# Performance work log

Measured on AMD Instinct MI355X. Metric: run time of the kernel, lower is better.

## Reference

```python
import jax, jax.numpy as jnp
import numpy as np

B, T, E, H = 4, 1024, 512, 8


def setup_inputs() -> dict:
    key = jax.random.key(0)
    ks = jax.random.split(key, 8)
    s = 1.0 / np.sqrt(E)
    return {
        "x": jax.random.normal(ks[0], (B, T, E), dtype=jnp.float32),
        "mask": jnp.zeros((B, T, T), dtype=jnp.float32),
        "Wk": jax.random.uniform(ks[1], (H * E, E), minval=-s, maxval=s, dtype=jnp.float32),
        "Wq": jax.random.uniform(ks[2], (H * E, E), minval=-s, maxval=s, dtype=jnp.float32),
        "Wv": jax.random.uniform(ks[3], (H * E, E), minval=-s, maxval=s, dtype=jnp.float32),
        "Wu": jax.random.uniform(ks[4], (E, H * E), minval=-s, maxval=s, dtype=jnp.float32),
        "bu": jnp.zeros((E,), dtype=jnp.float32),
        "heads": H,
    }


def reference(x, mask, Wk, Wq, Wv, Wu, bu, heads):
    b, t, e = x.shape
    h = heads
    # Projections: torch Linear computes x @ W.T; output features laid out as [h, e]
    k = (x @ Wk.T).reshape(b, t, h, e).transpose(0, 2, 1, 3)  # [b,h,t,e]
    q = (x @ Wq.T).reshape(b, t, h, e).transpose(0, 2, 1, 3)
    v = (x @ Wv.T).reshape(b, t, h, e).transpose(0, 2, 1, 3)
    dot = jnp.einsum("bhqe,bhke->bhqk", q, k) / jnp.sqrt(jnp.float32(e))
    # mask repeat_interleave over b*h == broadcast over heads; subtracted additively
    att = jax.nn.softmax(dot - mask[:, None, :, :], axis=-1)
    out = jnp.einsum("bhqk,bhke->bhqe", att, v)  # [b,h,t,e]
    out = out.transpose(0, 2, 1, 3).reshape(b, t, h * e)
    return out @ Wu.T + bu
```

## Files before the change

### kernel.cpp

```cpp
#include <hip/hip_runtime.h>
#include <hip/hip_bf16.h>


typedef short bf16x8 __attribute__((ext_vector_type(8)));
typedef float f32x4 __attribute__((ext_vector_type(4)));
typedef unsigned short u16x8 __attribute__((ext_vector_type(8)));

__device__ __forceinline__ unsigned short f2bf(float f) {
  unsigned int u = __float_as_uint(f);
  u += 0x7FFFu + ((u >> 16) & 1u);
  return (unsigned short)(u >> 16);
}
__device__ __forceinline__ float bf2f(unsigned short s) {
  return __uint_as_float(((unsigned int)s) << 16);
}

typedef const __attribute__((address_space(1))) unsigned int* gas1_t;
typedef __attribute__((address_space(3))) unsigned int* las3_t;

__device__ __forceinline__ void gload16(const unsigned short* g, unsigned short* l) {
  __builtin_amdgcn_global_load_lds((gas1_t)g, (las3_t)l, 16, 0, 0);
}

__device__ __forceinline__ void store_val(unsigned short* p, float v) { *p = f2bf(v); }
__device__ __forceinline__ void store_val(float* p, float v) { *p = v; }

template<typename OutT>
__global__ __launch_bounds__(512, 1) void gemm_bt2(
    const unsigned short* __restrict__ A, const unsigned short* __restrict__ B,
    OutT* __restrict__ C,
    int K, int lda, int ldb, int ldc, int zshift,
    long long sAb, long long sAh, long long sBb, long long sBh,
    long long sCb, long long sCh, float alpha)
{
  const int tid  = threadIdx.x;
  const int lane = tid & 63;
  const int wave = tid >> 6;
  const int l15 = lane & 15, lhi = lane >> 4;
  const int wm = wave >> 2, wn = wave & 3;

  const int nx = gridDim.x, nxy = gridDim.x * gridDim.y;
  const int nwg = nxy * gridDim.z;
  int flat = blockIdx.x + nx * blockIdx.y + nxy * blockIdx.z;
  flat = (flat & 7) * (nwg >> 3) + (flat >> 3);
  const int bz = flat / nxy;
  const int rem = flat - bz * nxy;
  const int by = rem / nx;
  const int bx = rem - by * nx;

  const int bb = bz >> zshift, hh = bz & ((1 << zshift) - 1);
  const long long m0 = (long long)by * 256;
  const long long n0 = (long long)bx * 256;

  const unsigned short* Ab = A + bb * sAb + hh * sAh;
  const unsigned short* Bb = B + bb * sBb + hh * sBh;

  __shared__ __align__(16) unsigned short lds[49152];

  const unsigned short* gA[2];
  const unsigned short* gB[2];
  int fidx[2];
#pragma unroll
  for (int c = 0; c < 2; ++c) {
    const int f = c * 8 + wave;
    fidx[c] = f;
    gA[c] = Ab + (size_t)(m0 + f * 16 + l15) * lda + lhi * 8;
    gB[c] = Bb + (size_t)(n0 + f * 16 + l15) * ldb + lhi * 8;
  }

  auto stage = [&](int n, int p) {
    unsigned short* dst = lds + p * 16384;
    const int ko = n * 32;
#pragma unroll
    for (int c = 0; c < 2; ++c) {
      gload16(gA[c] + ko, dst + fidx[c] * 512);
      gload16(gB[c] + ko, dst + 8192 + fidx[c] * 512);
    }
  };

  f32x4 acc[8][4];
#pragma unroll
  for (int m = 0; m < 8; ++m)
#pragma unroll
    for (int n = 0; n < 4; ++n) acc[m][n] = (f32x4){0.f, 0.f, 0.f, 0.f};

  const int nt = K >> 5;
  stage(0, 0);
  stage(1, 1);
  asm volatile("s_waitcnt vmcnt(4)" ::: "memory");
  __builtin_amdgcn_sched_barrier(0);
  __builtin_amdgcn_s_barrier();

  for (int t = 0; t < nt; ++t) {
    const bool pref = (t + 2 < nt);
    if (pref) stage(t + 2, (t + 2) % 3);
    const unsigned short* base = lds + (t % 3) * 16384;
    bf16x8 af[8], bf[4];
#pragma unroll
    for (int mf = 0; mf < 8; ++mf)
      af[mf] = *(const bf16x8*)(base + (wm * 8 + mf) * 512 + lane * 8);
#pragma unroll
    for (int nf = 0; nf < 4; ++nf)
      bf[nf] = *(const bf16x8*)(base + 8192 + (wn * 4 + nf) * 512 + lane * 8);
    __builtin_amdgcn_s_setprio(1);
#pragma unroll
    for (int mf = 0; mf < 8; ++mf)
#pragma unroll
      for (int nf = 0; nf < 4; ++nf)
        acc[mf][nf] = __builtin_amdgcn_mfma_f32_16x16x32_bf16(af[mf], bf[nf], acc[mf][nf], 0, 0, 0);
    __builtin_amdgcn_s_setprio(0);
    if (pref) asm volatile("s_waitcnt vmcnt(4)" ::: "memory");
    else      asm volatile("s_waitcnt vmcnt(0)" ::: "memory");
    __builtin_amdgcn_sched_barrier(0);
    __builtin_amdgcn_s_barrier();
    __builtin_amdgcn_sched_barrier(0);
  }

  OutT* Cb = C + bb * sCb + hh * sCh;
#pragma unroll
  for (int mf = 0; mf < 8; ++mf) {
#pragma unroll
    for (int nf = 0; nf < 4; ++nf) {
      const long long col = n0 + wn * 64 + nf * 16 + l15;
#pragma unroll
      for (int r = 0; r < 4; ++r) {
        const long long row = m0 + wm * 128 + mf * 16 + lhi * 4 + r;
        store_val(Cb + (size_t)row * ldc + col, acc[mf][nf][r] * alpha);
      }
    }
  }
}

__global__ __launch_bounds__(256) void reduce_kernel(
    const float* __restrict__ P, const float* __restrict__ bias,
    float* __restrict__ out)
{
  const int i = blockIdx.x * 256 + threadIdx.x;
  const int col4 = i & 127;
  const float4* p4 = (const float4*)P + i;
  float4 s = p4[0];
#pragma unroll
  for (int z = 1; z < 8; ++z) {
    float4 v = p4[(size_t)z * 524288];
    s.x += v.x; s.y += v.y; s.z += v.z; s.w += v.w;
  }
  float4 b = ((const float4*)bias)[col4];
  s.x += b.x; s.y += b.y; s.z += b.z; s.w += b.w;
  ((float4*)out)[i] = s;
}

__global__ __launch_bounds__(256) void cast5_kernel(
    const float* __restrict__ s0, const float* __restrict__ s1,
    const float* __restrict__ s2, const float* __restrict__ s3,
    const float* __restrict__ s4, unsigned short* __restrict__ dst)
{
  const int seg = blockIdx.x >> 11;
  const int off = (blockIdx.x & 2047) * 256 + threadIdx.x;
  const float* s = s0;
  if (seg == 1) s = s1; else if (seg == 2) s = s2;
  else if (seg == 3) s = s3; else if (seg == 4) s = s4;
  float4 v = ((const float4*)s)[off];
  ushort4 o;
  o.x = f2bf(v.x); o.y = f2bf(v.y); o.z = f2bf(v.z); o.w = f2bf(v.w);
  ((ushort4*)dst)[(size_t)seg * 524288 + off] = o;
}

__global__ __launch_bounds__(256) void softmax_kernel(
    unsigned short* __restrict__ S, const float* __restrict__ mask)
{
  const int wave = threadIdx.x >> 6;
  const int lane = threadIdx.x & 63;
  const long long row = (long long)blockIdx.x * 4 + wave;
  const int q = (int)(row & 1023);
  const int b = (int)(row >> 13);
  unsigned short* Srow = S + row * 1024;
  const float* mrow = mask + ((size_t)b * 1024 + q) * 1024;

  u16x8 sv0 = ((const u16x8*)Srow)[lane * 2];
  u16x8 sv1 = ((const u16x8*)Srow)[lane * 2 + 1];
  float mk[16];
  const float4* m4 = (const float4*)mrow + lane * 4;
#pragma unroll
  for (int t = 0; t < 4; ++t) {
    float4 v = m4[t];
    mk[t * 4 + 0] = v.x; mk[t * 4 + 1] = v.y; mk[t * 4 + 2] = v.z; mk[t * 4 + 3] = v.w;
  }

  float lg[16];
#pragma unroll
  for (int j = 0; j < 8; ++j) lg[j] = bf2f(sv0[j]) - mk[j];
#pragma unroll
  for (int j = 0; j < 8; ++j) lg[8 + j] = bf2f(sv1[j]) - mk[8 + j];

  float mx = lg[0];
#pragma unroll
  for (int j = 1; j < 16; ++j) mx = fmaxf(mx, lg[j]);
#pragma unroll
  for (int off = 32; off > 0; off >>= 1) mx = fmaxf(mx, __shfl_xor(mx, off));

  float ex[16], sm = 0.f;
#pragma unroll
  for (int j = 0; j < 16; ++j) { ex[j] = __expf(lg[j] - mx); sm += ex[j]; }
#pragma unroll
  for (int off = 32; off > 0; off >>= 1) sm += __shfl_xor(sm, off);
  const float rinv = 1.0f / sm;

  u16x8 o0, o1;
#pragma unroll
  for (int j = 0; j < 8; ++j) o0[j] = f2bf(ex[j] * rinv);
#pragma unroll
  for (int j = 0; j < 8; ++j) o1[j] = f2bf(ex[8 + j] * rinv);
  ((u16x8*)Srow)[lane * 2] = o0;
  ((u16x8*)Srow)[lane * 2 + 1] = o1;
}

extern "C" void kernel_launch(void* const* d_in, const int* in_sizes, int n_in,
                              void* d_out, int out_size, void* d_ws, size_t ws_size,
                              hipStream_t stream) {
  const float* x    = (const float*)d_in[0];
  const float* mask = (const float*)d_in[1];
  const float* Wk   = (const float*)d_in[2];
  const float* Wq   = (const float*)d_in[3];
  const float* Wv   = (const float*)d_in[4];
  const float* Wu   = (const float*)d_in[5];
  const float* bu   = (const float*)d_in[6];

  const size_t MB = 1024 * 1024;
  if (ws_size < 212 * MB) return;
  char* ws = (char*)d_ws;
  unsigned short* xb  = (unsigned short*)(ws + 0 * MB);
  unsigned short* Wqb = (unsigned short*)(ws + 4 * MB);
  unsigned short* Wkb = (unsigned short*)(ws + 8 * MB);
  unsigned short* Wvb = (unsigned short*)(ws + 12 * MB);
  unsigned short* Wub = (unsigned short*)(ws + 16 * MB);
  unsigned short* Qb  = (unsigned short*)(ws + 20 * MB);
  unsigned short* Kb  = (unsigned short*)(ws + 52 * MB);
  unsigned short* Vt  = (unsigned short*)(ws + 84 * MB);
  unsigned short* Sb  = (unsigned short*)(ws + 116 * MB);
  unsigned short* Ob  = (unsigned short*)(ws + 180 * MB);
  float* Pk = (float*)(ws + 20 * MB);

  cast5_kernel<<<5 * 2048, 256, 0, stream>>>(x, Wq, Wk, Wv, Wu, xb);

  gemm_bt2<unsigned short><<<dim3(16, 16, 2), 512, 0, stream>>>(
      xb, Wqb, Qb, 512, 512, 512, 4096, 0,
      0, 0, 2097152LL, 0, 16777216LL, 0, 1.0f);
  gemm_bt2<unsigned short><<<dim3(16, 16, 1), 512, 0, stream>>>(
      Wvb, xb, Vt, 512, 512, 512, 4096, 0, 0, 0, 0, 0, 0, 0, 1.0f);

  gemm_bt2<unsigned short><<<dim3(4, 4, 32), 512, 0, stream>>>(
      Qb, Kb, Sb, 512, 4096, 4096, 1024, 3,
      4194304LL, 512LL, 4194304LL, 512LL, 8388608LL, 1048576LL,
      0.044194173824159216f);

  softmax_kernel<<<8192, 256, 0, stream>>>(Sb, mask);

  gemm_bt2<unsigned short><<<dim3(2, 4, 32), 512, 0, stream>>>(
      Sb, Vt, Ob, 1024, 1024, 4096, 4096, 3,
      8388608LL, 1048576LL, 1024LL, 2097152LL, 4194304LL, 512LL, 1.0f);

  gemm_bt2<float><<<dim3(2, 16, 8), 512, 0, stream>>>(
      Ob, Wub, Pk, 512, 4096, 4096, 512, 0,
      512LL, 0, 512LL, 0, 2097152LL, 0, 1.0f);

  reduce_kernel<<<2048, 256, 0, stream>>>(Pk, bu, (float*)d_out);
}
```

Baseline: 250.4 us.

## Split GEMM main loop into two phases with 4-stage LDS ring

Moves the GEMM main loop from a 3-buffer LDS ring to a 4-buffer ring, growing LDS to 128KB. Each K-step now runs in two halves. The A-prefetch is issued after the first fragment reads and the B-prefetch after the second, with extra workgroup barriers and lgkmcnt waits between the halves. The aim is to interleave global-to-LDS loads with MFMA work and to hold fewer A fragments in registers at once. The cost is more barriers per iteration, and the larger LDS footprint may limit occupancy.

```diff
diff --git a/kernel.cpp b/kernel.cpp
--- a/kernel.cpp
+++ b/kernel.cpp
@@ -55,7 +55,7 @@
   const unsigned short* Ab = A + bb * sAb + hh * sAh;
   const unsigned short* Bb = B + bb * sBb + hh * sBh;
 
-  __shared__ __align__(16) unsigned short lds[49152];
+  __shared__ __align__(16) unsigned short lds[65536];
 
   const unsigned short* gA[2];
   const unsigned short* gB[2];
@@ -68,15 +68,18 @@
     gB[c] = Bb + (size_t)(n0 + f * 16 + l15) * ldb + lhi * 8;
   }
 
-  auto stage = [&](int n, int p) {
+  auto stageA = [&](int n, int p) {
     unsigned short* dst = lds + p * 16384;
     const int ko = n * 32;
 #pragma unroll
-    for (int c = 0; c < 2; ++c) {
-      gload16(gA[c] + ko, dst + fidx[c] * 512);
-      gload16(gB[c] + ko, dst + 8192 + fidx[c] * 512);
-    }
+    for (int c = 0; c < 2; ++c) gload16(gA[c] + ko, dst + fidx[c] * 512);
   };
+  auto stageB = [&](int n, int p) {
+    unsigned short* dst = lds + p * 16384 + 8192;
+    const int ko = n * 32;
+#pragma unroll
+    for (int c = 0; c < 2; ++c) gload16(gB[c] + ko, dst + fidx[c] * 512);
+  };
 
   f32x4 acc[8][4];
 #pragma unroll
@@ -85,29 +88,53 @@
     for (int n = 0; n < 4; ++n) acc[m][n] = (f32x4){0.f, 0.f, 0.f, 0.f};
 
   const int nt = K >> 5;
-  stage(0, 0);
-  stage(1, 1);
+  stageA(0, 0); stageB(0, 0);
+  stageA(1, 1); stageB(1, 1);
   asm volatile("s_waitcnt vmcnt(4)" ::: "memory");
   __builtin_amdgcn_sched_barrier(0);
   __builtin_amdgcn_s_barrier();
+  __builtin_amdgcn_sched_barrier(0);
 
   for (int t = 0; t < nt; ++t) {
+    const int p = t & 3;
+    const unsigned short* base = lds + p * 16384;
     const bool pref = (t + 2 < nt);
-    if (pref) stage(t + 2, (t + 2) % 3);
-    const unsigned short* base = lds + (t % 3) * 16384;
-    bf16x8 af[8], bf[4];
-#pragma unroll
-    for (int mf = 0; mf < 8; ++mf)
-      af[mf] = *(const bf16x8*)(base + (wm * 8 + mf) * 512 + lane * 8);
-#pragma unroll
-    for (int nf = 0; nf < 4; ++nf)
-      bf[nf] = *(const bf16x8*)(base + 8192 + (wn * 4 + nf) * 512 + lane * 8);
+    const int pd = (t + 2) & 3;
+
+    bf16x8 af[4], bf[4];
+#pragma unroll
+    for (int i = 0; i < 4; ++i)
+      af[i] = *(const bf16x8*)(base + (wm * 8 + i) * 512 + lane * 8);
+#pragma unroll
+    for (int i = 0; i < 4; ++i)
+      bf[i] = *(const bf16x8*)(base + 8192 + (wn * 4 + i) * 512 + lane * 8);
+    if (pref) stageA(t + 2, pd);
+    __builtin_amdgcn_s_barrier();
+    asm volatile("s_waitcnt lgkmcnt(0)" ::: "memory");
+    __builtin_amdgcn_sched_barrier(0);
     __builtin_amdgcn_s_setprio(1);
 #pragma unroll
-    for (int mf = 0; mf < 8; ++mf)
+    for (int mf = 0; mf < 4; ++mf)
 #pragma unroll
       for (int nf = 0; nf < 4; ++nf)
         acc[mf][nf] = __builtin_amdgcn_mfma_f32_16x16x32_bf16(af[mf], bf[nf], acc[mf][nf], 0, 0, 0);
+    __builtin_amdgcn_s_setprio(0);
+    __builtin_amdgcn_s_barrier();
+    __builtin_amdgcn_sched_barrier(0);
+
+#pragma unroll
+    for (int i = 0; i < 4; ++i)
+      af[i] = *(const bf16x8*)(base + (wm * 8 + 4 + i) * 512 + lane * 8);
+    if (pref) stageB(t + 2, pd);
+    __builtin_amdgcn_s_barrier();
+    asm volatile("s_waitcnt lgkmcnt(0)" ::: "memory");
+    __builtin_amdgcn_sched_barrier(0);
+    __builtin_amdgcn_s_setprio(1);
+#pragma unroll
+    for (int mf = 0; mf < 4; ++mf)
+#pragma unroll
+      for (int nf = 0; nf < 4; ++nf)
+        acc[mf + 4][nf] = __builtin_amdgcn_mfma_f32_16x16x32_bf16(af[mf], bf[nf], acc[mf + 4][nf], 0, 0, 0);
     __builtin_amdgcn_s_setprio(0);
     if (pref) asm volatile("s_waitcnt vmcnt(4)" ::: "memory");
     else      asm volatile("s_waitcnt vmcnt(0)" ::: "memory");
```

Result: no change. 252.9 us (+1.0%).

## Double-buffer K=64 GEMM stages with interleaved prefetch across four sub-phases

Applied to the files above, without the earlier changes.

The bf16 MFMA GEMM mainloop moves from a triple-buffered K=32 step to a double-buffered K=64 step. Each iteration is split into four sub-phases: it loads A fragments per pair of M-tiles, issues pieces of the next tile's global-to-LDS loads between sub-phases, and places partial vmcnt waits and a barrier after each phase. The aim is to halve the loop-iteration and barrier overhead per unit of K and to spread global loads across the MFMA work. In exchange it uses more LDS (128 KB), adds four barriers per iteration, and the waitcnt bookkeeping is fragile.

```diff
diff --git a/kernel.cpp b/kernel.cpp
--- a/kernel.cpp
+++ b/kernel.cpp
@@ -55,28 +55,23 @@
   const unsigned short* Ab = A + bb * sAb + hh * sAh;
   const unsigned short* Bb = B + bb * sBb + hh * sBh;
 
-  __shared__ __align__(16) unsigned short lds[49152];
-
-  const unsigned short* gA[2];
-  const unsigned short* gB[2];
-  int fidx[2];
-#pragma unroll
-  for (int c = 0; c < 2; ++c) {
-    const int f = c * 8 + wave;
-    fidx[c] = f;
-    gA[c] = Ab + (size_t)(m0 + f * 16 + l15) * lda + lhi * 8;
-    gB[c] = Bb + (size_t)(n0 + f * 16 + l15) * ldb + lhi * 8;
-  }
-
-  auto stage = [&](int n, int p) {
-    unsigned short* dst = lds + p * 16384;
-    const int ko = n * 32;
-#pragma unroll
-    for (int c = 0; c < 2; ++c) {
-      gload16(gA[c] + ko, dst + fidx[c] * 512);
-      gload16(gB[c] + ko, dst + 8192 + fidx[c] * 512);
-    }
+  __shared__ __align__(16) unsigned short lds[65536];
+
+  const int w = wave;
+  const unsigned short* pB = Bb + (size_t)(n0 + (w >> 1) * 16 + l15) * ldb
+                                + (w & 1) * 32 + lhi * 8;
+  const unsigned short* pA = Ab + (size_t)(m0 + ((w >> 1) & 1) * 16 + (w >> 2) * 128 + l15) * lda
+                                + (w & 1) * 32 + lhi * 8;
+  const int abase = ((w >> 1) & 1) * 2 + (w >> 2) * 16 + (w & 1);
+
+  auto stageBH = [&](int h, int k0, int bsel) {
+    unsigned short* dst = lds + bsel * 32768 + 16384;
+    gload16(pB + (size_t)(h * 128) * ldb + k0,      dst + (16 * h + w) * 512);
+    gload16(pB + (size_t)(h * 128 + 64) * ldb + k0, dst + (16 * h + 8 + w) * 512);
   };
+  auto stageAC = [&](int j, int k0, int bsel) {
+    gload16(pA + (size_t)(j * 32) * lda + k0, lds + bsel * 32768 + (4 * j + abase) * 512);
+  };
 
   f32x4 acc[8][4];
 #pragma unroll
@@ -84,36 +79,63 @@
 #pragma unroll
     for (int n = 0; n < 4; ++n) acc[m][n] = (f32x4){0.f, 0.f, 0.f, 0.f};
 
-  const int nt = K >> 5;
-  stage(0, 0);
-  stage(1, 1);
-  asm volatile("s_waitcnt vmcnt(4)" ::: "memory");
+  const int nt = K >> 6;
+  stageBH(0, 0, 0); stageBH(1, 0, 0);
+  stageAC(0, 0, 0); stageAC(1, 0, 0); stageAC(2, 0, 0); stageAC(3, 0, 0);
+  asm volatile("s_waitcnt vmcnt(0)" ::: "memory");
   __builtin_amdgcn_sched_barrier(0);
   __builtin_amdgcn_s_barrier();
+  __builtin_amdgcn_sched_barrier(0);
 
   for (int t = 0; t < nt; ++t) {
-    const bool pref = (t + 2 < nt);
-    if (pref) stage(t + 2, (t + 2) % 3);
-    const unsigned short* base = lds + (t % 3) * 16384;
-    bf16x8 af[8], bf[4];
-#pragma unroll
-    for (int mf = 0; mf < 8; ++mf)
-      af[mf] = *(const bf16x8*)(base + (wm * 8 + mf) * 512 + lane * 8);
-#pragma unroll
-    for (int nf = 0; nf < 4; ++nf)
-      bf[nf] = *(const bf16x8*)(base + 8192 + (wn * 4 + nf) * 512 + lane * 8);
-    __builtin_amdgcn_s_setprio(1);
-#pragma unroll
-    for (int mf = 0; mf < 8; ++mf)
-#pragma unroll
-      for (int nf = 0; nf < 4; ++nf)
-        acc[mf][nf] = __builtin_amdgcn_mfma_f32_16x16x32_bf16(af[mf], bf[nf], acc[mf][nf], 0, 0, 0);
-    __builtin_amdgcn_s_setprio(0);
-    if (pref) asm volatile("s_waitcnt vmcnt(4)" ::: "memory");
-    else      asm volatile("s_waitcnt vmcnt(0)" ::: "memory");
-    __builtin_amdgcn_sched_barrier(0);
-    __builtin_amdgcn_s_barrier();
-    __builtin_amdgcn_sched_barrier(0);
+    const int bsel = t & 1;
+    const unsigned short* Abuf = lds + bsel * 32768;
+    const unsigned short* Bbuf = Abuf + 16384;
+    const bool pref = (t + 1 < nt);
+    const int nk = (t + 1) * 64;
+    const int nb = bsel ^ 1;
+
+    bf16x8 bfr[4][2];
+#pragma unroll
+    for (int p = 0; p < 4; ++p) {
+      bf16x8 af[2][2];
+#pragma unroll
+      for (int i = 0; i < 2; ++i)
+#pragma unroll
+        for (int ks = 0; ks < 2; ++ks)
+          af[i][ks] = *(const bf16x8*)(Abuf + ((wm * 8 + 2 * p + i) * 2 + ks) * 512 + lane * 8);
+      if (p == 0) {
+#pragma unroll
+        for (int nf = 0; nf < 4; ++nf)
+#pragma unroll
+          for (int ks = 0; ks < 2; ++ks)
+            bfr[nf][ks] = *(const bf16x8*)(Bbuf + ((wn * 4 + nf) * 2 + ks) * 512 + lane * 8);
+      }
+      if (pref) {
+        if (p == 0) stageBH(0, nk, nb);
+        if (p == 1) stageBH(1, nk, nb);
+        if (p == 2) { stageAC(0, nk, nb); stageAC(1, nk, nb); }
+        if (p == 3) { stageAC(2, nk, nb); stageAC(3, nk, nb); }
+      }
+      __builtin_amdgcn_s_setprio(1);
+#pragma unroll
+      for (int i = 0; i < 2; ++i)
+#pragma unroll
+        for (int nf = 0; nf < 4; ++nf)
+#pragma unroll
+          for (int ks = 0; ks < 2; ++ks)
+            acc[2 * p + i][nf] = __builtin_amdgcn_mfma_f32_16x16x32_bf16(
+                af[i][ks], bfr[nf][ks], acc[2 * p + i][nf], 0, 0, 0);
+      __builtin_amdgcn_s_setprio(0);
+      if (p == 1) {
+        if (pref) asm volatile("s_waitcnt vmcnt(4)" ::: "memory");
+        else      asm volatile("s_waitcnt vmcnt(0)" ::: "memory");
+      }
+      if (p == 3 && pref) asm volatile("s_waitcnt vmcnt(2)" ::: "memory");
+      __builtin_amdgcn_sched_barrier(0);
+      __builtin_amdgcn_s_barrier();
+      __builtin_amdgcn_sched_barrier(0);
+    }
   }
 
   OutT* Cb = C + bb * sCb + hh * sCh;
```

Result: no change. 248.8 us (-0.7%).

## Fold Wq and Wk into per-head bilinear matrix to skip separate Q and K projections

Applied to the files above, without the earlier changes.

Instead of projecting x into Q and K separately, the code precomputes for each head a 512x512 matrix N_h = Wq_h^T Wk_h (via a transpose kernel and a small batched GEMM), computes xM = x N_h, and forms scores as xM · x^T. This replaces two large projections (x times 4096x512 each) with one projection plus a small weight GEMM, and the score GEMM now reads x directly as the K operand. It adds a transpose kernel and an extra bf16 rounding of N_h, which changes numerical error.

```diff
diff --git a/kernel.cpp b/kernel.cpp
--- a/kernel.cpp
+++ b/kernel.cpp
@@ -129,6 +129,33 @@
       }
     }
   }
+}
+
+__global__ __launch_bounds__(256) void wtrans_kernel(
+    const unsigned short* __restrict__ Wq, const unsigned short* __restrict__ Wk,
+    unsigned short* __restrict__ Wqt, unsigned short* __restrict__ Wkt)
+{
+  __shared__ unsigned short t[64][72];
+  const int k0 = blockIdx.x * 64;
+  const int i0 = blockIdx.y * 64;
+  const int hz = blockIdx.z;
+  const int h = hz & 7;
+  const unsigned short* src = (hz < 8) ? Wq : Wk;
+  unsigned short* dst = (hz < 8) ? Wqt : Wkt;
+  const int tid = threadIdx.x;
+  const int r = tid >> 2, c16 = (tid & 3) * 16;
+  const unsigned short* sp = src + (size_t)(h * 512 + k0 + r) * 512 + i0 + c16;
+  u16x8 v0 = *(const u16x8*)sp;
+  u16x8 v1 = *(const u16x8*)(sp + 8);
+#pragma unroll
+  for (int j = 0; j < 8; ++j) { t[r][c16 + j] = v0[j]; t[r][c16 + 8 + j] = v1[j]; }
+  __syncthreads();
+  unsigned short o[16];
+#pragma unroll
+  for (int j = 0; j < 16; ++j) o[j] = t[c16 + j][r];
+  unsigned short* dp = dst + (size_t)h * 262144 + (size_t)(i0 + r) * 512 + k0 + c16;
+  *(u16x8*)dp = *(u16x8*)o;
+  *(u16x8*)(dp + 8) = *(u16x8*)(o + 8);
 }
 
 __global__ __launch_bounds__(256) void reduce_kernel(
@@ -226,41 +253,57 @@
   const float* bu   = (const float*)d_in[6];
 
   const size_t MB = 1024 * 1024;
-  if (ws_size < 212 * MB) return;
+  if (ws_size < 192 * MB) return;
   char* ws = (char*)d_ws;
   unsigned short* xb  = (unsigned short*)(ws + 0 * MB);
   unsigned short* Wqb = (unsigned short*)(ws + 4 * MB);
   unsigned short* Wkb = (unsigned short*)(ws + 8 * MB);
   unsigned short* Wvb = (unsigned short*)(ws + 12 * MB);
   unsigned short* Wub = (unsigned short*)(ws + 16 * MB);
-  unsigned short* Qb  = (unsigned short*)(ws + 20 * MB);
-  unsigned short* Kb  = (unsigned short*)(ws + 52 * MB);
-  unsigned short* Vt  = (unsigned short*)(ws + 84 * MB);
-  unsigned short* Sb  = (unsigned short*)(ws + 116 * MB);
-  unsigned short* Ob  = (unsigned short*)(ws + 180 * MB);
-  float* Pk = (float*)(ws + 20 * MB);
+  unsigned short* Wqt = (unsigned short*)(ws + 20 * MB);
+  unsigned short* Wkt = (unsigned short*)(ws + 24 * MB);
+  unsigned short* Nh  = (unsigned short*)(ws + 28 * MB);
+  unsigned short* xM  = (unsigned short*)(ws + 32 * MB);
+  unsigned short* Vt  = (unsigned short*)(ws + 64 * MB);
+  unsigned short* Sb  = (unsigned short*)(ws + 96 * MB);
+  unsigned short* Ob  = (unsigned short*)(ws + 160 * MB);
+  float* Pk = (float*)(ws + 96 * MB);
 
   cast5_kernel<<<5 * 2048, 256, 0, stream>>>(x, Wq, Wk, Wv, Wu, xb);
 
-  gemm_bt2<unsigned short><<<dim3(16, 16, 2), 512, 0, stream>>>(
-      xb, Wqb, Qb, 512, 512, 512, 4096, 0,
-      0, 0, 2097152LL, 0, 16777216LL, 0, 1.0f);
+  wtrans_kernel<<<dim3(8, 8, 16), 256, 0, stream>>>(Wqb, Wkb, Wqt, Wkt);
+
+  gemm_bt2<unsigned short><<<dim3(2, 2, 8), 512, 0, stream>>>(
+      Wkt, Wqt, Nh,
+      512, 512, 512, 512, 0,
+      262144LL, 0, 262144LL, 0, 262144LL, 0, 1.0f);
+
+  gemm_bt2<unsigned short><<<dim3(2, 16, 8), 512, 0, stream>>>(
+      xb, Nh, xM,
+      512, 512, 512, 4096, 0,
+      0, 0, 262144LL, 0, 512LL, 0, 1.0f);
+
   gemm_bt2<unsigned short><<<dim3(16, 16, 1), 512, 0, stream>>>(
-      Wvb, xb, Vt, 512, 512, 512, 4096, 0, 0, 0, 0, 0, 0, 0, 1.0f);
+      Wvb, xb, Vt,
+      512, 512, 512, 4096, 0,
+      0, 0, 0, 0, 0, 0, 1.0f);
 
   gemm_bt2<unsigned short><<<dim3(4, 4, 32), 512, 0, stream>>>(
-      Qb, Kb, Sb, 512, 4096, 4096, 1024, 3,
-      4194304LL, 512LL, 4194304LL, 512LL, 8388608LL, 1048576LL,
+      xM, xb, Sb,
+      512, 4096, 512, 1024, 3,
+      4194304LL, 512LL, 524288LL, 0, 8388608LL, 1048576LL,
       0.044194173824159216f);
 
   softmax_kernel<<<8192, 256, 0, stream>>>(Sb, mask);
 
   gemm_bt2<unsigned short><<<dim3(2, 4, 32), 512, 0, stream>>>(
-      Sb, Vt, Ob, 1024, 1024, 4096, 4096, 3,
+      Sb, Vt, Ob,
+      1024, 1024, 4096, 4096, 3,
       8388608LL, 1048576LL, 1024LL, 2097152LL, 4194304LL, 512LL, 1.0f);
 
   gemm_bt2<float><<<dim3(2, 16, 8), 512, 0, stream>>>(
-      Ob, Wub, Pk, 512, 4096, 4096, 512, 0,
+      Ob, Wub, Pk,
+      512, 4096, 4096, 512, 0,
       512LL, 0, 512LL, 0, 2097152LL, 0, 1.0f);
 
   reduce_kernel<<<2048, 256, 0, stream>>>(Pk, bu, (float*)d_out);
```

Result: faster. 242.4 us (-3.2%).
